# Optimization experiments

Measured on AMD Instinct MI355X. Metric: run time of the kernel, lower is better.

Reference implementation:

```python
import jax, jax.numpy as jnp
import numpy as np

B, DIM, H, W = 8, 128, 64, 64
HEADS = 8
NUMS = DIM // HEADS   # 16
OUT = 256

def setup_inputs() -> dict:
    key = jax.random.key(0)
    k1, k2, k3, k4, k5 = jax.random.split(key, 5)
    x = jax.random.normal(k1, (B, DIM, H, W), dtype=jnp.float32)
    # per-group 1x1 conv (num_heads -> 1): weight [nums, heads], bias [nums]
    W1 = jax.random.normal(k2, (NUMS, HEADS), dtype=jnp.float32) * (1.0 / np.sqrt(HEADS))
    b1 = jax.random.normal(k3, (NUMS,), dtype=jnp.float32) * 0.01
    # final 1x1 conv (nums*dim -> out_dim): weight [out, nums*dim], bias [out]
    W2 = jax.random.normal(k4, (OUT, NUMS * DIM), dtype=jnp.float32) * (1.0 / np.sqrt(NUMS * DIM))
    b2 = jax.random.normal(k5, (OUT,), dtype=jnp.float32) * 0.01
    return {"x": x, "W1": W1, "b1": b1, "W2": W2, "b2": b2}

def reference(x, W1, b1, W2, b2):
    B_, C, H_, W_ = x.shape
    # split channels into nums groups of num_heads: [B, nums, heads, H, W]
    xg = x.reshape(B_, NUMS, HEADS, H_, W_)
    # per-group 1x1 conv to 1 channel + ReLU -> attention maps [B, nums, H, W]
    fm = jax.nn.relu(jnp.einsum('bghxy,gh->bgxy', xg, W1) + b1[None, :, None, None])
    # broadcast-multiply each map against full x, concat -> [B, nums*dim, H, W]
    feat = (fm[:, :, None, :, :] * x[:, None, :, :, :]).reshape(B_, NUMS * C, H_, W_)
    # final 1x1 conv -> [B, out_dim, H, W]
    out = jnp.einsum('bcxy,oc->boxy', feat, W2) + b2[None, :, None, None]
    return out
```

## Files before the change

kernel.cpp:

```cpp
#include <hip/hip_runtime.h>

typedef float f32x4 __attribute__((ext_vector_type(4)));
typedef int   i32x4 __attribute__((ext_vector_type(4)));
typedef unsigned int u32;

#define HW_N  4096
#define C_N   128
#define G_N   16
#define K_N   2048
#define O_N   256
#define BN    128

typedef const __attribute__((address_space(1))) u32 gbl_u32;
typedef __attribute__((address_space(3))) u32 lds_u32;

__device__ __forceinline__ u32 pack4(float a, float b, float c, float d, float inv) {
  int q0 = (int)rintf(a * inv), q1 = (int)rintf(b * inv);
  int q2 = (int)rintf(c * inv), q3 = (int)rintf(d * inv);
  return (u32)(q0 & 255) | ((u32)(q1 & 255) << 8) |
         ((u32)(q2 & 255) << 16) | ((u32)(q3 & 255) << 24);
}

__global__ void w2q_k(const float* __restrict__ W2, char* __restrict__ w2q,
                      float* __restrict__ sw) {
  int o = blockIdx.x;
  int l = threadIdx.x;
  const f32x4* rp = reinterpret_cast<const f32x4*>(W2 + (size_t)o * K_N + l * 32);
  float v[32]; float am = 0.f;
#pragma unroll
  for (int q = 0; q < 8; ++q) {
    f32x4 t = rp[q];
#pragma unroll
    for (int j = 0; j < 4; ++j) { v[q * 4 + j] = t[j]; am = fmaxf(am, fabsf(t[j])); }
  }
#pragma unroll
  for (int s = 1; s < 64; s <<= 1) am = fmaxf(am, __shfl_xor(am, s, 64));
  am = fmaxf(am, 1e-30f);
  float inv = 127.0f / am;
  if (l == 0) sw[o] = am / 127.0f;
#pragma unroll
  for (int c = 0; c < 2; ++c) {
    int k0 = l * 32 + c * 16;
    u32 pk[4];
#pragma unroll
    for (int q = 0; q < 4; ++q)
      pk[q] = pack4(v[c * 16 + q * 4 + 0], v[c * 16 + q * 4 + 1],
                    v[c * 16 + q * 4 + 2], v[c * 16 + q * 4 + 3], inv);
    int g   = k0 >> 7;
    int ks2 = (k0 >> 6) & 1;
    int lif = (o & 15) + ((k0 >> 4) & 3) * 16;
    *reinterpret_cast<i32x4*>(w2q + (size_t)g * 32768 + (o >> 4) * 2048 +
                              ks2 * 1024 + lif * 16) = *reinterpret_cast<i32x4*>(pk);
  }
}

__launch_bounds__(256, 2)
__global__ void ccattn_main_k(const float* __restrict__ x,
                              const float* __restrict__ W1,
                              const float* __restrict__ b1,
                              const char* __restrict__ w2q,
                              const float* __restrict__ sw,
                              const float* __restrict__ b2,
                              float* __restrict__ out) {
  __shared__ __align__(16) char Albs[2][16384];
  __shared__ char  qxT[BN * 128];
  __shared__ float fmT[G_N][BN];
  __shared__ float sxT[BN];
  __shared__ float lmax[2][BN];

  const int tid = threadIdx.x;
  const int bid = blockIdx.x;
  const int mt  = bid >> 8;
  const int pt  = bid & 255;
  const int b   = pt >> 5;
  const int px0 = (pt & 31) * BN;

  const int w = tid >> 6;
  const int l = tid & 63;

  auto stage = [&](int g, int slot) {
    const char* src = w2q + (size_t)g * 32768 + mt * 16384 + w * 4096 + l * 16;
    char* dst = &Albs[slot][w * 4096];
#pragma unroll
    for (int r = 0; r < 4; ++r)
      __builtin_amdgcn_global_load_lds((gbl_u32*)(src + r * 1024),
                                       (lds_u32*)(dst + r * 1024), 16, 0, 0);
  };
  stage(0, 0);
  stage(1, 1);

  const float* xb = x + (size_t)b * C_N * HW_N + px0;

  const int px    = tid & 127;
  const int chalf = tid >> 7;
  float v[8][8];
  {
    float am = 0.f;
#pragma unroll
    for (int gg = 0; gg < 8; ++gg) {
      const int g  = chalf * 8 + gg;
      const int c0 = g * 8;
      float s = b1[g];
#pragma unroll
      for (int j = 0; j < 8; ++j) {
        float t = xb[(size_t)(c0 + j) * HW_N + px];
        v[gg][j] = t;
        s += t * W1[g * 8 + j];
        am = fmaxf(am, fabsf(t));
      }
      fmT[g][px] = fmaxf(s, 0.0f);
    }
    lmax[chalf][px] = am;
  }
  __syncthreads();

  {
    float amax = fmaxf(fmaxf(lmax[0][px], lmax[1][px]), 1e-30f);
    float inv  = 127.0f / amax;
    if (!chalf) sxT[px] = amax / 127.0f;
#pragma unroll
    for (int gr = 0; gr < 4; ++gr) {
      u32 pk[4];
#pragma unroll
      for (int q = 0; q < 4; ++q) {
        const int gg = gr * 2 + (q >> 1);
        const int j0 = (q & 1) * 4;
        pk[q] = pack4(v[gg][j0], v[gg][j0 + 1], v[gg][j0 + 2], v[gg][j0 + 3], inv);
      }
      int gidx = chalf * 4 + gr;
      int byte = px * 128 + ((gidx ^ (px & 7)) << 4);
      *reinterpret_cast<i32x4*>(qxT + byte) = *reinterpret_cast<i32x4*>(pk);
    }
  }
  __syncthreads();

  const int wm = w & 1;
  const int wn = w >> 1;
  const int lc = l & 15;
  const int lk = l >> 4;

  i32x4 bfr[2][4];
#pragma unroll
  for (int ks2 = 0; ks2 < 2; ++ks2)
#pragma unroll
    for (int nf = 0; nf < 4; ++nf) {
      int p    = wn * 64 + nf * 16 + lc;
      int gidx = ks2 * 4 + lk;
      int byte = p * 128 + ((gidx ^ (p & 7)) << 4);
      bfr[ks2][nf] = *reinterpret_cast<const i32x4*>(qxT + byte);
    }

  f32x4 acc[4][4];
#pragma unroll
  for (int mf = 0; mf < 4; ++mf)
#pragma unroll
    for (int nf = 0; nf < 4; ++nf) acc[mf][nf] = (f32x4){0.f, 0.f, 0.f, 0.f};

#pragma unroll 1
  for (int g = 0; g < 16; ++g) {
    const char* ab = &Albs[g & 1][(size_t)wm * 8192];
    i32x4 afr[8];
#pragma unroll
    for (int mf = 0; mf < 4; ++mf) {
      afr[mf * 2]     = *reinterpret_cast<const i32x4*>(ab + mf * 2048 + l * 16);
      afr[mf * 2 + 1] = *reinterpret_cast<const i32x4*>(ab + mf * 2048 + 1024 + l * 16);
    }
    float sn[4];
#pragma unroll
    for (int nf = 0; nf < 4; ++nf) sn[nf] = fmT[g][wn * 64 + nf * 16 + lc];

    __builtin_amdgcn_s_setprio(1);
#pragma unroll
    for (int nf = 0; nf < 4; ++nf) {
      i32x4 P[4];
#pragma unroll
      for (int mf = 0; mf < 4; ++mf)
        P[mf] = __builtin_amdgcn_mfma_i32_16x16x64_i8(
            afr[mf * 2], bfr[0][nf], (i32x4){0, 0, 0, 0}, 0, 0, 0);
#pragma unroll
      for (int mf = 0; mf < 4; ++mf)
        P[mf] = __builtin_amdgcn_mfma_i32_16x16x64_i8(
            afr[mf * 2 + 1], bfr[1][nf], P[mf], 0, 0, 0);
#pragma unroll
      for (int mf = 0; mf < 4; ++mf) {
#pragma unroll
        for (int i = 0; i < 4; ++i)
          acc[mf][nf][i] += sn[nf] * (float)P[mf][i];
      }
    }
    __builtin_amdgcn_s_setprio(0);

    __syncthreads();
    if (g + 2 < 16) stage(g + 2, g & 1);
  }

  float sxv[4];
#pragma unroll
  for (int nf = 0; nf < 4; ++nf) sxv[nf] = sxT[wn * 64 + nf * 16 + lc];
  float* outb = out + (size_t)b * O_N * HW_N + px0;
#pragma unroll
  for (int mf = 0; mf < 4; ++mf) {
    int o0 = mt * 128 + wm * 64 + mf * 16 + lk * 4;
#pragma unroll
    for (int i = 0; i < 4; ++i) {
      float so   = sw[o0 + i];
      float bias = b2[o0 + i];
#pragma unroll
      for (int nf = 0; nf < 4; ++nf) {
        int p = wn * 64 + nf * 16 + lc;
        outb[(size_t)(o0 + i) * HW_N + p] = acc[mf][nf][i] * so * sxv[nf] + bias;
      }
    }
  }
}

extern "C" void kernel_launch(void* const* d_in, const int* in_sizes, int n_in,
                              void* d_out, int out_size, void* d_ws, size_t ws_size,
                              hipStream_t stream) {
  const float* x  = (const float*)d_in[0];
  const float* W1 = (const float*)d_in[1];
  const float* b1 = (const float*)d_in[2];
  const float* W2 = (const float*)d_in[3];
  const float* b2 = (const float*)d_in[4];
  float* out = (float*)d_out;
  char*  w2q = (char*)d_ws;
  float* sw  = (float*)((char*)d_ws + 524288);

  w2q_k<<<256, 64, 0, stream>>>(W2, w2q, sw);
  ccattn_main_k<<<512, 256, 0, stream>>>(x, W1, b1, w2q, sw, b2, out);
}
```

Measured before the change: 36.73 us.

## Triple-buffer W2 tiles and software-pipeline int8 MFMA with scaled accumulation

The LDS staging of quantized W2 tiles moves from a double to a triple buffer. Each group iteration now issues the next prefetch right after one explicit waitcnt and barrier, instead of after a trailing __syncthreads. The float rescale-and-accumulate of the previous group's int32 MFMA products is deferred one iteration, so it can overlap the current group's MFMAs and the prefetch. The cost is more LDS per block, which threatens two blocks per CU, and a live P[4][4] int32 buffer that raises register pressure.

```diff
diff --git a/kernel.cpp b/kernel.cpp
--- a/kernel.cpp
+++ b/kernel.cpp
@@ -62,7 +62,7 @@
                               const float* __restrict__ sw,
                               const float* __restrict__ b2,
                               float* __restrict__ out) {
-  __shared__ __align__(16) char Albs[2][16384];
+  __shared__ __align__(16) char Albs[3][16384];
   __shared__ char  qxT[BN * 128];
   __shared__ float fmT[G_N][BN];
   __shared__ float sxT[BN];
@@ -156,43 +156,65 @@
 #pragma unroll
     for (int nf = 0; nf < 4; ++nf) acc[mf][nf] = (f32x4){0.f, 0.f, 0.f, 0.f};
 
+  const int aoff = wm * 8192 + l * 16;
+
+  i32x4 afr[8];
+  i32x4 P[4][4];
+  float snP[4];
+
 #pragma unroll 1
   for (int g = 0; g < 16; ++g) {
-    const char* ab = &Albs[g & 1][(size_t)wm * 8192];
-    i32x4 afr[8];
+    asm volatile("s_waitcnt lgkmcnt(0)" ::: "memory");
+    asm volatile("s_waitcnt vmcnt(0)" ::: "memory");
+    __builtin_amdgcn_s_barrier();
+    const char* ab = &Albs[g % 3][0];
 #pragma unroll
     for (int mf = 0; mf < 4; ++mf) {
-      afr[mf * 2]     = *reinterpret_cast<const i32x4*>(ab + mf * 2048 + l * 16);
-      afr[mf * 2 + 1] = *reinterpret_cast<const i32x4*>(ab + mf * 2048 + 1024 + l * 16);
-    }
-    float sn[4];
-#pragma unroll
-    for (int nf = 0; nf < 4; ++nf) sn[nf] = fmT[g][wn * 64 + nf * 16 + lc];
+      afr[mf * 2]     = *reinterpret_cast<const i32x4*>(ab + mf * 2048 + aoff);
+      afr[mf * 2 + 1] = *reinterpret_cast<const i32x4*>(ab + mf * 2048 + 1024 + aoff);
+    }
+    float snC[4];
+#pragma unroll
+    for (int nf = 0; nf < 4; ++nf) snC[nf] = fmT[g][wn * 64 + nf * 16 + lc];
+    if (g + 2 < 16) stage(g + 2, (g + 2) % 3);
+
+    if (g > 0) {
+#pragma unroll
+      for (int mf = 0; mf < 4; ++mf)
+#pragma unroll
+        for (int nf = 0; nf < 4; ++nf) {
+#pragma unroll
+          for (int i = 0; i < 4; ++i)
+            acc[mf][nf][i] += snP[nf] * (float)P[mf][nf][i];
+        }
+    }
+#pragma unroll
+    for (int nf = 0; nf < 4; ++nf) snP[nf] = snC[nf];
 
     __builtin_amdgcn_s_setprio(1);
 #pragma unroll
+    for (int nf = 0; nf < 4; ++nf)
+#pragma unroll
+      for (int mf = 0; mf < 4; ++mf)
+        P[mf][nf] = __builtin_amdgcn_mfma_i32_16x16x64_i8(
+            afr[mf * 2], bfr[0][nf], (i32x4){0, 0, 0, 0}, 0, 0, 0);
+#pragma unroll
+    for (int nf = 0; nf < 4; ++nf)
+#pragma unroll
+      for (int mf = 0; mf < 4; ++mf)
+        P[mf][nf] = __builtin_amdgcn_mfma_i32_16x16x64_i8(
+            afr[mf * 2 + 1], bfr[1][nf], P[mf][nf], 0, 0, 0);
+    __builtin_amdgcn_s_setprio(0);
+  }
+
+#pragma unroll
+  for (int mf = 0; mf < 4; ++mf)
+#pragma unroll
     for (int nf = 0; nf < 4; ++nf) {
-      i32x4 P[4];
-#pragma unroll
-      for (int mf = 0; mf < 4; ++mf)
-        P[mf] = __builtin_amdgcn_mfma_i32_16x16x64_i8(
-            afr[mf * 2], bfr[0][nf], (i32x4){0, 0, 0, 0}, 0, 0, 0);
-#pragma unroll
-      for (int mf = 0; mf < 4; ++mf)
-        P[mf] = __builtin_amdgcn_mfma_i32_16x16x64_i8(
-            afr[mf * 2 + 1], bfr[1][nf], P[mf], 0, 0, 0);
-#pragma unroll
-      for (int mf = 0; mf < 4; ++mf) {
-#pragma unroll
-        for (int i = 0; i < 4; ++i)
-          acc[mf][nf][i] += sn[nf] * (float)P[mf][i];
-      }
-    }
-    __builtin_amdgcn_s_setprio(0);
-
-    __syncthreads();
-    if (g + 2 < 16) stage(g + 2, g & 1);
-  }
+#pragma unroll
+      for (int i = 0; i < 4; ++i)
+        acc[mf][nf][i] += snP[nf] * (float)P[mf][nf][i];
+    }
 
   float sxv[4];
 #pragma unroll
```

Result: faster. 34.88 us (-5.0%).
